# Optimization experiments

Measured on AMD Instinct MI355X. Metric: run time of the kernel, lower is better.

Reference implementation:

```python
import jax, jax.numpy as jnp
import numpy as np

EPS = 1e-5


def layer_norm(x, g, b):
    mu = jnp.mean(x, axis=-1, keepdims=True)
    var = jnp.var(x, axis=-1, keepdims=True)
    return (x - mu) * jax.lax.rsqrt(var + EPS) * g + b


def setup_inputs() -> dict:
    key = jax.random.key(0)
    ks = jax.random.split(key, 10)
    B, N, D, H, DFF = 4, 2048, 384, 6, 2048
    s = lambda fan: 1.0 / np.sqrt(fan)
    return {
        "x": jax.random.normal(ks[0], (B, N, D), dtype=jnp.float32),
        "norm_g": jnp.ones((D,), jnp.float32),
        "norm_b": jnp.zeros((D,), jnp.float32),
        "w_qkv": jax.random.uniform(ks[1], (D, 3 * D), jnp.float32, -s(D), s(D)),
        "b_qkv": jax.random.uniform(ks[2], (3 * D,), jnp.float32, -s(D), s(D)),
        "w1": jax.random.uniform(ks[3], (D, DFF), jnp.float32, -s(D), s(D)),
        "b1": jax.random.uniform(ks[4], (DFF,), jnp.float32, -s(D), s(D)),
        "w2": jax.random.uniform(ks[5], (DFF, D), jnp.float32, -s(DFF), s(DFF)),
        "b2": jax.random.uniform(ks[6], (D,), jnp.float32, -s(DFF), s(DFF)),
    }


def reference(x, norm_g, norm_b, w_qkv, b_qkv, w1, b1, w2, b2):
    H = 6
    B, N, D = x.shape
    hd = D // H
    scale = hd ** -0.5

    # --- attention (pre-norm, shared LayerNorm params) ---
    out = layer_norm(x, norm_g, norm_b)
    qkv = out @ w_qkv + b_qkv                     # [B, N, 3D]
    q, k, v = jnp.split(qkv, 3, axis=-1)
    to_heads = lambda t: t.reshape(B, N, H, hd).transpose(0, 2, 1, 3)  # b h n d
    q, k, v = to_heads(q), to_heads(k), to_heads(v)
    scores = jnp.einsum('bhid,bhjd->bhij', q, k) * scale
    attn = jax.nn.softmax(scores, axis=-1)        # dropout is identity in eval
    att = jnp.einsum('bhij,bhjd->bhid', attn, v)  # [B, H, N, hd]
    att = att.transpose(0, 2, 1, 3).reshape(B, N, D)
    x2 = x + att

    # --- MLP (same shared LayerNorm) ---
    y = layer_norm(x2, norm_g, norm_b)
    h = jax.nn.gelu(y @ w1 + b1, approximate=False)  # torch F.gelu exact
    mlp = h @ w2 + b2
    return x2 + mlp
```

## Files before the change

### kernel.cpp

```cpp
#include <hip/hip_runtime.h>
#include <cstdint>
#include <cstddef>

#define DEV static __device__ __forceinline__

typedef __attribute__((ext_vector_type(8))) short short8;
typedef __attribute__((ext_vector_type(4))) float f32x4;
typedef __attribute__((ext_vector_type(16))) float f32x16;
typedef __attribute__((ext_vector_type(4))) unsigned short u16x4;
typedef __attribute__((ext_vector_type(2))) unsigned short u16x2;

constexpr int kB = 4, kN = 2048, kD = 384, kH = 6, kDFF = 2048;
constexpr int kM = kB * kN;
constexpr int kBH = kB * kH;
constexpr float kQPre = 0.18033688011112042f;

DEV float exp2fast(float f) { return __builtin_amdgcn_exp2f(f); }

DEV unsigned short f2b(float f) {
  union { float fp; uint32_t u; } v; v.fp = f;
  return (unsigned short)((v.u + 0x7fffu + ((v.u >> 16) & 1u)) >> 16);
}

DEV void gload16(const unsigned short* g, unsigned short* l) {
  __builtin_amdgcn_global_load_lds(
      (const __attribute__((address_space(1))) unsigned int*)g,
      (__attribute__((address_space(3))) unsigned int*)l, 16, 0, 0);
}

DEV float gelu_fast(float x) {
  float t = exp2fast(x * (2.3022081f + 0.1029432f * x * x));
  return x - x * __builtin_amdgcn_rcpf(t + 1.0f);
}

__global__ __launch_bounds__(256) void k_pre(
    const float* __restrict__ wqkv, unsigned short* __restrict__ wqkvT,
    const float* __restrict__ w1,   unsigned short* __restrict__ w1T,
    const float* __restrict__ w2,   unsigned short* __restrict__ w2T,
    const float* __restrict__ x, const float* __restrict__ g,
    const float* __restrict__ bta, unsigned short* __restrict__ y) {
  const int tid = threadIdx.x;
  if (blockIdx.x >= 492) {
    int row  = (blockIdx.x - 492) * 4 + (tid >> 6);
    int lane = tid & 63;
    const float* xr = x + (size_t)row * kD;
    float4 a = *(const float4*)(xr + lane * 4);
    float2 c = *(const float2*)(xr + 256 + lane * 2);
    float s  = a.x + a.y + a.z + a.w + c.x + c.y;
    float ss = a.x*a.x + a.y*a.y + a.z*a.z + a.w*a.w + c.x*c.x + c.y*c.y;
#pragma unroll
    for (int m = 1; m < 64; m <<= 1) {
      s  += __shfl_xor(s,  m, 64);
      ss += __shfl_xor(ss, m, 64);
    }
    float mean = s * (1.0f / kD);
    float var  = ss * (1.0f / kD) - mean * mean;
    float r = rsqrtf(var + 1e-5f);
    float4 g4 = *(const float4*)(g + lane * 4);
    float2 g2 = *(const float2*)(g + 256 + lane * 2);
    float4 b4 = *(const float4*)(bta + lane * 4);
    float2 b2 = *(const float2*)(bta + 256 + lane * 2);
    unsigned short* yr = y + (size_t)row * kD;
    u16x4 o4;
    o4[0] = f2b((a.x - mean) * r * g4.x + b4.x);
    o4[1] = f2b((a.y - mean) * r * g4.y + b4.y);
    o4[2] = f2b((a.z - mean) * r * g4.z + b4.z);
    o4[3] = f2b((a.w - mean) * r * g4.w + b4.w);
    *(u16x4*)(yr + lane * 4) = o4;
    u16x2 o2;
    o2[0] = f2b((c.x - mean) * r * g2.x + b2.x);
    o2[1] = f2b((c.y - mean) * r * g2.y + b2.y);
    *(u16x2*)(yr + 256 + lane * 2) = o2;
    return;
  }
  __shared__ unsigned short t[64][66];
  int idx = blockIdx.x;
  const float* w; unsigned short* wT; int K, Nn, nbk;
  if (idx < 108)      { w = wqkv; wT = wqkvT; K = 384;  Nn = 1152; nbk = 6; }
  else if (idx < 300) { w = w1;   wT = w1T;   K = 384;  Nn = 2048; nbk = 6;  idx -= 108; }
  else                { w = w2;   wT = w2T;   K = 2048; Nn = 384;  nbk = 32; idx -= 300; }
  const int bk = idx % nbk, bn = idx / nbk;
  const int k0 = bk << 6, n0 = bn << 6;
  const int cl = tid & 63, rw = tid >> 6;
#pragma unroll
  for (int it = 0; it < 16; ++it) {
    int kk = it * 4 + rw;
    t[cl][kk] = f2b(w[(size_t)(k0 + kk) * Nn + n0 + cl]);
  }
  __syncthreads();
  const int kq = (tid & 15) << 2;
  const int nr = tid >> 4;
#pragma unroll
  for (int it = 0; it < 4; ++it) {
    int nn = it * 16 + nr;
    u16x4 v;
    v[0] = t[nn][kq]; v[1] = t[nn][kq + 1]; v[2] = t[nn][kq + 2]; v[3] = t[nn][kq + 3];
    *(u16x4*)&wT[(size_t)(n0 + nn) * K + k0 + kq] = v;
  }
}

__global__ __launch_bounds__(256) void k_layernorm(
    const float* __restrict__ x, const float* __restrict__ g,
    const float* __restrict__ bta, unsigned short* __restrict__ y) {
  int row  = blockIdx.x * 4 + (threadIdx.x >> 6);
  int lane = threadIdx.x & 63;
  const float* xr = x + (size_t)row * kD;
  float4 a = *(const float4*)(xr + lane * 4);
  float2 c = *(const float2*)(xr + 256 + lane * 2);
  float s  = a.x + a.y + a.z + a.w + c.x + c.y;
  float ss = a.x*a.x + a.y*a.y + a.z*a.z + a.w*a.w + c.x*c.x + c.y*c.y;
#pragma unroll
  for (int m = 1; m < 64; m <<= 1) {
    s  += __shfl_xor(s,  m, 64);
    ss += __shfl_xor(ss, m, 64);
  }
  float mean = s * (1.0f / kD);
  float var  = ss * (1.0f / kD) - mean * mean;
  float r = rsqrtf(var + 1e-5f);
  float4 g4 = *(const float4*)(g + lane * 4);
  float2 g2 = *(const float2*)(g + 256 + lane * 2);
  float4 b4 = *(const float4*)(bta + lane * 4);
  float2 b2 = *(const float2*)(bta + 256 + lane * 2);
  unsigned short* yr = y + (size_t)row * kD;
  u16x4 o4;
  o4[0] = f2b((a.x - mean) * r * g4.x + b4.x);
  o4[1] = f2b((a.y - mean) * r * g4.y + b4.y);
  o4[2] = f2b((a.z - mean) * r * g4.z + b4.z);
  o4[3] = f2b((a.w - mean) * r * g4.w + b4.w);
  *(u16x4*)(yr + lane * 4) = o4;
  u16x2 o2;
  o2[0] = f2b((c.x - mean) * r * g2.x + b2.x);
  o2[1] = f2b((c.y - mean) * r * g2.y + b2.y);
  *(u16x2*)(yr + 256 + lane * 2) = o2;
}

template <int MODE, int TM>
__global__ __launch_bounds__(256) void k_gemm(
    const unsigned short* __restrict__ A, const unsigned short* __restrict__ Bt,
    const float* __restrict__ bias, int K, int Nn, int nbm,
    unsigned short* __restrict__ oq, unsigned short* __restrict__ okk,
    unsigned short* __restrict__ ov, unsigned short* __restrict__ oh,
    const float* __restrict__ res, float* __restrict__ out) {
  constexpr int FI = (TM >= 64) ? TM / 64 : 1;
  constexpr int FJ = (TM >= 64) ? 2 : 1;
  __shared__ unsigned short lA[2][TM * 32];
  __shared__ unsigned short lB[2][128 * 32];
  const int tid = threadIdx.x, wid = tid >> 6, lane = tid & 63;
  const int bm = blockIdx.x % nbm, bn = blockIdx.x / nbm;
  const int m0 = bm * TM, n0 = bn * 128;
  const int wr = (TM >= 64) ? (wid >> 1) : 0;
  const int wc = (TM >= 64) ? (wid & 1) : wid;
  const int wmo = wr * (TM >> 1);
  const int wno = wc * (FJ * 32);
  const int l31 = lane & 31, lh = lane >> 5;
  const int gsw = (l31 >> 1) & 3;

  f32x16 acc[FI][FJ];
#pragma unroll
  for (int i = 0; i < FI; i++)
#pragma unroll
    for (int j = 0; j < FJ; j++)
#pragma unroll
      for (int r = 0; r < 16; r++) acc[i][j][r] = 0.f;

  const int srow = (lane >> 2);
  const int scc  = (lane & 3) << 3;

  auto stage = [&](int buf, int k0) {
    if constexpr (TM >= 64) {
#pragma unroll
      for (int p = 0; p < TM / 64; p++) {
        int row = ((wid + (p << 2)) << 4) + srow;
        int sl  = ((lane & 3) ^ ((row >> 1) & 3)) << 3;
        gload16(A + (size_t)(m0 + row) * K + k0 + sl, &lA[buf][(row << 5) + scc]);
      }
    } else {
      if (tid < TM * 4) {
        int row = tid >> 2;
        int sl  = ((tid & 3) ^ ((row >> 1) & 3)) << 3;
        gload16(A + (size_t)(m0 + row) * K + k0 + sl,
                &lA[buf][(row << 5) + ((tid & 3) << 3)]);
      }
    }
#pragma unroll
    for (int p = 0; p < 2; p++) {
      int row = ((wid + (p << 2)) << 4) + srow;
      int sl  = ((lane & 3) ^ ((row >> 1) & 3)) << 3;
      gload16(Bt + (size_t)(n0 + row) * K + k0 + sl, &lB[buf][(row << 5) + scc]);
    }
  };

  stage(0, 0);

  const int nkt = K >> 5;
  for (int kt = 0; kt < nkt; ++kt) {
    const int cur = kt & 1;
    __syncthreads();
    if (kt + 1 < nkt) stage(cur ^ 1, (kt + 1) << 5);
    short8 af[FI][2], bf[FJ][2];
#pragma unroll
    for (int i = 0; i < FI; i++)
#pragma unroll
      for (int ks = 0; ks < 2; ks++)
        af[i][ks] = *(const short8*)&lA[cur][(wmo + (i << 5) + l31) * 32 +
                                            ((((ks << 1) + lh) ^ gsw) << 3)];
#pragma unroll
    for (int j = 0; j < FJ; j++)
#pragma unroll
      for (int ks = 0; ks < 2; ks++)
        bf[j][ks] = *(const short8*)&lB[cur][(wno + (j << 5) + l31) * 32 +
                                            ((((ks << 1) + lh) ^ gsw) << 3)];
#pragma unroll
    for (int i = 0; i < FI; i++)
#pragma unroll
      for (int j = 0; j < FJ; j++)
#pragma unroll
        for (int ks = 0; ks < 2; ks++)
          acc[i][j] = __builtin_amdgcn_mfma_f32_32x32x16_bf16(af[i][ks], bf[j][ks],
                                                              acc[i][j], 0, 0, 0);
  }

#pragma unroll
  for (int i = 0; i < FI; i++) {
#pragma unroll
    for (int j = 0; j < FJ; j++) {
      int col = n0 + wno + (j << 5) + l31;
      float bv = bias[col];
#pragma unroll
      for (int reg = 0; reg < 16; ++reg) {
        int m = m0 + wmo + (i << 5) + (reg & 3) + ((reg >> 2) << 3) + (lh << 2);
        float cvl = acc[i][j][reg] + bv;
        if (MODE == 0) {
          int bI = m >> 11, nI = m & 2047;
          if (col < 384) {
            int hh = col >> 6, dd = col & 63;
            oq[(((size_t)bI * kH + hh) * kN + nI) * 64 + dd] = f2b(cvl * kQPre);
          } else if (col < 768) {
            int c2 = col - 384; int hh = c2 >> 6, dd = c2 & 63;
            okk[(((size_t)bI * kH + hh) * kN + nI) * 64 + dd] = f2b(cvl);
          } else {
            int c2 = col - 768; int hh = c2 >> 6, dd = c2 & 63;
            ov[(((size_t)bI * kH + hh) * 64 + dd) * kN + nI] = f2b(cvl);
          }
        } else if (MODE == 1) {
          oh[(size_t)m * kDFF + col] = f2b(gelu_fast(cvl));
        } else {
          size_t idx = (size_t)m * kD + col;
          out[idx] = res[idx] + cvl;
        }
      }
    }
  }
}

__global__ __launch_bounds__(256) void k_attn(
    const unsigned short* __restrict__ Q, const unsigned short* __restrict__ Kg,
    const unsigned short* __restrict__ Vt, const float* __restrict__ x,
    float* __restrict__ x2) {
  __shared__ unsigned short lK[2][64 * 64];
  __shared__ unsigned short lV[2][64 * 64];
  __shared__ unsigned short lP[4][16 * 64];
  const int tid = threadIdx.x, wid = tid >> 6, lane = tid & 63;
  const int swz = (blockIdx.x & 7) * (gridDim.x >> 3) + (blockIdx.x >> 3);
  const int bh = swz >> 5, qt = swz & 31;
  const int b = bh / kH, h = bh - b * kH;
  const unsigned short* Qp = Q  + (size_t)bh * kN * 64;
  const unsigned short* Kp = Kg + (size_t)bh * kN * 64;
  const unsigned short* Vp = Vt + (size_t)bh * 64 * kN;
  const int lr16 = lane & 15, lq = lane >> 4;
  const int q0w = qt * 64 + wid * 16;
  const int rsw = (lr16 & 7) << 3;

  const int sr  = ((wid << 3) + (lane >> 3));
  const int scc = (lane & 7) << 3;

  short8 qf[2];
#pragma unroll
  for (int ks = 0; ks < 2; ++ks)
    qf[ks] = *(const short8*)(Qp + (size_t)(q0w + lr16) * 64 + ks * 32 + lq * 8);

  const short8 ones = {0x3F80, 0x3F80, 0x3F80, 0x3F80, 0x3F80, 0x3F80, 0x3F80, 0x3F80};
  f32x4 o[4], o_l;
#pragma unroll
  for (int df = 0; df < 4; ++df) o[df] = f32x4{0.f, 0.f, 0.f, 0.f};
  o_l = f32x4{0.f, 0.f, 0.f, 0.f};

  auto stage = [&](int buf, int t) {
#pragma unroll
    for (int p = 0; p < 2; p++) {
      int r = sr + (p << 5);
      int sl = ((lane & 7) ^ (r & 7)) << 3;
      gload16(Kp + (size_t)(t * 64 + r) * 64 + sl, &lK[buf][(r << 6) + scc]);
      gload16(Vp + (size_t)r * kN + t * 64 + sl,   &lV[buf][(r << 6) + scc]);
    }
  };

  stage(0, 0);

  constexpr int kNT = kN / 64;
  for (int t = 0; t < kNT; ++t) {
    const int cur = t & 1;
    __syncthreads();
    if (t + 1 < kNT) stage(cur ^ 1, t + 1);

    f32x4 s4[4];
#pragma unroll
    for (int j = 0; j < 4; j++) {
      s4[j] = f32x4{0.f, 0.f, 0.f, 0.f};
#pragma unroll
      for (int ks = 0; ks < 2; ks++) {
        short8 kf = *(const short8*)&lK[cur][((j << 4) + lr16) * 64 + ((ks * 32 + (lq << 3)) ^ rsw)];
        s4[j] = __builtin_amdgcn_mfma_f32_16x16x32_bf16(kf, qf[ks], s4[j], 0, 0, 0);
      }
    }

#pragma unroll
    for (int j = 0; j < 4; j++) {
      float p0 = exp2fast(s4[j][0]);
      float p1 = exp2fast(s4[j][1]);
      float p2 = exp2fast(s4[j][2]);
      float p3 = exp2fast(s4[j][3]);
      uint32_t w0, w1;
      asm("v_cvt_pk_bf16_f32 %0, %1, %2" : "=v"(w0) : "v"(p0), "v"(p1));
      asm("v_cvt_pk_bf16_f32 %0, %1, %2" : "=v"(w1) : "v"(p2), "v"(p3));
      int kvb = (j << 4) + (lq << 2);
      uint2 wv; wv.x = w0; wv.y = w1;
      *(uint2*)&lP[wid][(lr16 << 6) + (kvb ^ rsw)] = wv;
    }

    short8 pa[2];
#pragma unroll
    for (int ks = 0; ks < 2; ks++)
      pa[ks] = *(const short8*)&lP[wid][(lr16 << 6) + ((ks * 32 + (lq << 3)) ^ rsw)];
#pragma unroll
    for (int ks = 0; ks < 2; ks++)
      o_l = __builtin_amdgcn_mfma_f32_16x16x32_bf16(pa[ks], ones, o_l, 0, 0, 0);
#pragma unroll
    for (int df = 0; df < 4; df++) {
#pragma unroll
      for (int ks = 0; ks < 2; ks++) {
        short8 vf = *(const short8*)&lV[cur][((df << 4) + lr16) * 64 + ((ks * 32 + (lq << 3)) ^ rsw)];
        o[df] = __builtin_amdgcn_mfma_f32_16x16x32_bf16(pa[ks], vf, o[df], 0, 0, 0);
      }
    }
  }

  float inv[4];
#pragma unroll
  for (int rr = 0; rr < 4; rr++) inv[rr] = __builtin_amdgcn_rcpf(o_l[rr]);
#pragma unroll
  for (int df = 0; df < 4; df++)
#pragma unroll
    for (int rr = 0; rr < 4; rr++) {
      int row  = q0w + (lq << 2) + rr;
      int colD = h * 64 + (df << 4) + lr16;
      size_t idx = ((size_t)(b * kN + row)) * kD + colD;
      x2[idx] = x[idx] + o[df][rr] * inv[rr];
    }
}

extern "C" void kernel_launch(void* const* d_in, const int* in_sizes, int n_in,
                              void* d_out, int out_size, void* d_ws, size_t ws_size,
                              hipStream_t stream) {
  const float* x    = (const float*)d_in[0];
  const float* ng   = (const float*)d_in[1];
  const float* nb   = (const float*)d_in[2];
  const float* wqkv = (const float*)d_in[3];
  const float* bqkv = (const float*)d_in[4];
  const float* w1   = (const float*)d_in[5];
  const float* b1   = (const float*)d_in[6];
  const float* w2   = (const float*)d_in[7];
  const float* b2   = (const float*)d_in[8];
  float* out = (float*)d_out;

  char* p = (char*)d_ws;
  auto take = [&](size_t bytes) -> char* {
    char* r = p; p += (bytes + 255) & ~(size_t)255; return r;
  };
  unsigned short* y     = (unsigned short*)take((size_t)kM * kD * 2);
  unsigned short* wqkvT = (unsigned short*)take((size_t)3 * kD * kD * 2);
  unsigned short* w1T   = (unsigned short*)take((size_t)kDFF * kD * 2);
  unsigned short* w2T   = (unsigned short*)take((size_t)kD * kDFF * 2);
  unsigned short* Qw    = (unsigned short*)take((size_t)kM * kD * 2);
  unsigned short* Kw    = (unsigned short*)take((size_t)kM * kD * 2);
  unsigned short* Vtw   = (unsigned short*)take((size_t)kM * kD * 2);
  float*          x2    = (float*)take((size_t)kM * kD * 4);
  unsigned short* hbuf  = (unsigned short*)take((size_t)kM * kDFF * 2);

  k_pre<<<492 + kM / 4, 256, 0, stream>>>(wqkv, wqkvT, w1, w1T, w2, w2T,
                                          x, ng, nb, y);
  k_gemm<0, 64><<<128 * 9, 256, 0, stream>>>(y, wqkvT, bqkv, kD, 3 * kD, 128,
                                             Qw, Kw, Vtw, nullptr, nullptr, nullptr);
  k_attn<<<kBH * 32, 256, 0, stream>>>(Qw, Kw, Vtw, x, x2);
  k_layernorm<<<kM / 4, 256, 0, stream>>>(x2, ng, nb, y);
  k_gemm<1, 128><<<64 * 16, 256, 0, stream>>>(y, w1T, b1, kD, kDFF, 64,
                                              nullptr, nullptr, nullptr, hbuf, nullptr, nullptr);
  k_gemm<2, 32><<<256 * 3, 256, 0, stream>>>(hbuf, w2T, b2, kDFF, kD, 256,
                                             nullptr, nullptr, nullptr, nullptr, x2, out);
}
```

Measured before the change: 150.6 us.

## Switch attention to 32x32x16 MFMA with split-KV across waves and LDS reduction

The attention kernel is reorganised so each wave computes a 32-query by 32-key tile with 32x32x16 bf16 MFMA instructions. Waves are split into two query halves and two KV halves, and the two KV-half partial outputs and row sums are combined through LDS at the end. This is meant to improve MFMA efficiency and halve the per-wave K/V fragment reads. In exchange it doubles the P staging buffer in LDS and adds a final reduction with extra barriers.

```diff
diff --git a/kernel.cpp b/kernel.cpp
--- a/kernel.cpp
+++ b/kernel.cpp
@@ -259,7 +259,7 @@
     float* __restrict__ x2) {
   __shared__ unsigned short lK[2][64 * 64];
   __shared__ unsigned short lV[2][64 * 64];
-  __shared__ unsigned short lP[4][16 * 64];
+  __shared__ unsigned short lP[4][32 * 64];
   const int tid = threadIdx.x, wid = tid >> 6, lane = tid & 63;
   const int swz = (blockIdx.x & 7) * (gridDim.x >> 3) + (blockIdx.x >> 3);
   const int bh = swz >> 5, qt = swz & 31;
@@ -267,23 +267,27 @@
   const unsigned short* Qp = Q  + (size_t)bh * kN * 64;
   const unsigned short* Kp = Kg + (size_t)bh * kN * 64;
   const unsigned short* Vp = Vt + (size_t)bh * 64 * kN;
-  const int lr16 = lane & 15, lq = lane >> 4;
-  const int q0w = qt * 64 + wid * 16;
-  const int rsw = (lr16 & 7) << 3;
+  const int l31 = lane & 31, lh = lane >> 5;
+  const int qh = wid & 1, kvh = wid >> 1;
+  const int q0 = qt * 64;
+  const int psw = l31 & 7;
 
   const int sr  = ((wid << 3) + (lane >> 3));
   const int scc = (lane & 7) << 3;
 
-  short8 qf[2];
-#pragma unroll
-  for (int ks = 0; ks < 2; ++ks)
-    qf[ks] = *(const short8*)(Qp + (size_t)(q0w + lr16) * 64 + ks * 32 + lq * 8);
+  short8 qb[4];
+#pragma unroll
+  for (int ks = 0; ks < 4; ++ks)
+    qb[ks] = *(const short8*)(Qp + (size_t)(q0 + qh * 32 + l31) * 64 + ks * 16 + lh * 8);
 
   const short8 ones = {0x3F80, 0x3F80, 0x3F80, 0x3F80, 0x3F80, 0x3F80, 0x3F80, 0x3F80};
-  f32x4 o[4], o_l;
-#pragma unroll
-  for (int df = 0; df < 4; ++df) o[df] = f32x4{0.f, 0.f, 0.f, 0.f};
-  o_l = f32x4{0.f, 0.f, 0.f, 0.f};
+  f32x16 o[2], ol;
+#pragma unroll
+  for (int db = 0; db < 2; ++db)
+#pragma unroll
+    for (int r = 0; r < 16; r++) o[db][r] = 0.f;
+#pragma unroll
+  for (int r = 0; r < 16; r++) ol[r] = 0.f;
 
   auto stage = [&](int buf, int t) {
 #pragma unroll
@@ -303,60 +307,76 @@
     __syncthreads();
     if (t + 1 < kNT) stage(cur ^ 1, t + 1);
 
-    f32x4 s4[4];
-#pragma unroll
-    for (int j = 0; j < 4; j++) {
-      s4[j] = f32x4{0.f, 0.f, 0.f, 0.f};
-#pragma unroll
-      for (int ks = 0; ks < 2; ks++) {
-        short8 kf = *(const short8*)&lK[cur][((j << 4) + lr16) * 64 + ((ks * 32 + (lq << 3)) ^ rsw)];
-        s4[j] = __builtin_amdgcn_mfma_f32_16x16x32_bf16(kf, qf[ks], s4[j], 0, 0, 0);
-      }
-    }
-
-#pragma unroll
-    for (int j = 0; j < 4; j++) {
-      float p0 = exp2fast(s4[j][0]);
-      float p1 = exp2fast(s4[j][1]);
-      float p2 = exp2fast(s4[j][2]);
-      float p3 = exp2fast(s4[j][3]);
+    f32x16 s;
+#pragma unroll
+    for (int r = 0; r < 16; r++) s[r] = 0.f;
+#pragma unroll
+    for (int ks = 0; ks < 4; ++ks) {
+      int krow = kvh * 32 + l31;
+      short8 kf = *(const short8*)&lK[cur][(krow << 6) +
+                                          ((((ks << 1) + lh) ^ psw) << 3)];
+      s = __builtin_amdgcn_mfma_f32_32x32x16_bf16(kf, qb[ks], s, 0, 0, 0);
+    }
+
+#pragma unroll
+    for (int g = 0; g < 4; ++g) {
+      float p0 = exp2fast(s[4 * g + 0]);
+      float p1 = exp2fast(s[4 * g + 1]);
+      float p2 = exp2fast(s[4 * g + 2]);
+      float p3 = exp2fast(s[4 * g + 3]);
       uint32_t w0, w1;
       asm("v_cvt_pk_bf16_f32 %0, %1, %2" : "=v"(w0) : "v"(p0), "v"(p1));
       asm("v_cvt_pk_bf16_f32 %0, %1, %2" : "=v"(w1) : "v"(p2), "v"(p3));
-      int kvb = (j << 4) + (lq << 2);
       uint2 wv; wv.x = w0; wv.y = w1;
-      *(uint2*)&lP[wid][(lr16 << 6) + (kvb ^ rsw)] = wv;
+      *(uint2*)&lP[wid][(l31 << 6) + ((g ^ psw) << 3) + (lh << 2)] = wv;
     }
 
     short8 pa[2];
 #pragma unroll
-    for (int ks = 0; ks < 2; ks++)
-      pa[ks] = *(const short8*)&lP[wid][(lr16 << 6) + ((ks * 32 + (lq << 3)) ^ rsw)];
-#pragma unroll
-    for (int ks = 0; ks < 2; ks++)
-      o_l = __builtin_amdgcn_mfma_f32_16x16x32_bf16(pa[ks], ones, o_l, 0, 0, 0);
-#pragma unroll
-    for (int df = 0; df < 4; df++) {
-#pragma unroll
-      for (int ks = 0; ks < 2; ks++) {
-        short8 vf = *(const short8*)&lV[cur][((df << 4) + lr16) * 64 + ((ks * 32 + (lq << 3)) ^ rsw)];
-        o[df] = __builtin_amdgcn_mfma_f32_16x16x32_bf16(pa[ks], vf, o[df], 0, 0, 0);
+    for (int ks = 0; ks < 2; ++ks)
+      pa[ks] = *(const short8*)&lP[wid][(l31 << 6) + ((((ks << 1) + lh) ^ psw) << 3)];
+#pragma unroll
+    for (int ks = 0; ks < 2; ++ks)
+      ol = __builtin_amdgcn_mfma_f32_32x32x16_bf16(pa[ks], ones, ol, 0, 0, 0);
+#pragma unroll
+    for (int db = 0; db < 2; ++db) {
+      int vrow = db * 32 + l31;
+#pragma unroll
+      for (int ks = 0; ks < 2; ++ks) {
+        short8 vb = *(const short8*)&lV[cur][(vrow << 6) +
+                      ((((kvh << 2) + (ks << 1) + lh) ^ (vrow & 7)) << 3)];
+        o[db] = __builtin_amdgcn_mfma_f32_32x32x16_bf16(pa[ks], vb, o[db], 0, 0, 0);
       }
     }
   }
 
-  float inv[4];
-#pragma unroll
-  for (int rr = 0; rr < 4; rr++) inv[rr] = __builtin_amdgcn_rcpf(o_l[rr]);
-#pragma unroll
-  for (int df = 0; df < 4; df++)
-#pragma unroll
-    for (int rr = 0; rr < 4; rr++) {
-      int row  = q0w + (lq << 2) + rr;
-      int colD = h * 64 + (df << 4) + lr16;
-      size_t idx = ((size_t)(b * kN + row)) * kD + colD;
-      x2[idx] = x[idx] + o[df][rr] * inv[rr];
-    }
+  __syncthreads();
+  float* fb = (float*)&lP[0][0] + qh * 2048;
+  float* lb = (float*)&lK[0][0] + qh * 32;
+  if (kvh == 1) {
+#pragma unroll
+    for (int reg = 0; reg < 16; ++reg) {
+      int row = (reg & 3) + ((reg >> 2) << 3) + (lh << 2);
+      fb[row * 64 +      l31] = o[0][reg];
+      fb[row * 64 + 32 + l31] = o[1][reg];
+      if (l31 == 0) lb[row] = ol[reg];
+    }
+  }
+  __syncthreads();
+  if (kvh == 0) {
+#pragma unroll
+    for (int reg = 0; reg < 16; ++reg) {
+      int row = (reg & 3) + ((reg >> 2) << 3) + (lh << 2);
+      float inv = __builtin_amdgcn_rcpf(ol[reg] + lb[row]);
+      int gq = q0 + qh * 32 + row;
+#pragma unroll
+      for (int db = 0; db < 2; ++db) {
+        float val = o[db][reg] + fb[row * 64 + db * 32 + l31];
+        size_t idx = ((size_t)(b * kN + gq)) * kD + h * 64 + db * 32 + l31;
+        x2[idx] = x[idx] + val * inv;
+      }
+    }
+  }
 }
 
 extern "C" void kernel_launch(void* const* d_in, const int* in_sizes, int n_in,
```

Result: no change. 148.9 us (-1.2%).
